# Optimization experiments

Hardware: AMD Instinct MI355X
Metric: run time of the kernel (lower is better)

The kernel has to match this reference:

```python
import jax, jax.numpy as jnp
import numpy as np

HEADS = 8
DIM_HEAD = 64
KERNEL = 33


def setup_inputs() -> dict:
    key = jax.random.key(0)
    k1, k2, k3 = jax.random.split(key, 3)
    b, n, dim = 8, 1315, 512
    x = jax.random.normal(k1, (b, n, dim), dtype=jnp.float32)
    w_qkv = jax.random.normal(k2, (dim, 3 * HEADS * DIM_HEAD), dtype=jnp.float32) * 0.02
    w_res = jax.random.normal(k3, (HEADS, 1, KERNEL, 1), dtype=jnp.float32) * 0.02
    return {"x": x, "w_qkv": w_qkv, "w_res": w_res,
            "target_num": 265, "neighbor_num": 25, "global_num": 1}


def reference(x, w_qkv, w_res, target_num, neighbor_num, global_num):
    b, n, _ = x.shape
    h, d = HEADS, DIM_HEAD
    scale = d ** -0.5
    num_image = target_num + neighbor_num + global_num

    qkv = x @ w_qkv                                   # [b, n, 3*h*d]
    q, k, v = jnp.split(qkv, 3, axis=-1)
    to_bhnd = lambda t: t.reshape(b, n, h, d).transpose(0, 2, 1, 3)
    q, k, v = map(to_bhnd, (q, k, v))                 # [b, h, n, d]
    q = q * scale

    q_img, k_img = q[:, :, :num_image], k[:, :, :num_image]
    q_gene, k_gene = q[:, :, num_image:], k[:, :, num_image:]

    cross_attn_image = jnp.einsum('bhid,bhjd->bhij', q_img, k_gene)   # [b,h,ni,ng]
    attn_gene = jnp.einsum('bhid,bhjd->bhij', q_gene, k_gene)          # [b,h,ng,ng]
    cross_attn_gene = jnp.einsum('bhid,bhjd->bhij', q_gene, k_img)     # [b,h,ng,ni]
    attn_image = jnp.einsum('bhid,bhjd->bhij', q_img, k_img)           # [b,h,ni,ni]

    # 'full' mode: softmax cross_attn_image first, then concatenated softmaxes
    cross_attn_image = jax.nn.softmax(cross_attn_image, axis=-1)
    attn_image_pathways = jax.nn.softmax(
        jnp.concatenate((cross_attn_image, attn_image), axis=-1), axis=-1)  # [b,h,ni,n]
    attn_gene_histology = jax.nn.softmax(
        jnp.concatenate((attn_gene, cross_attn_gene), axis=-1), axis=-1)    # [b,h,ng,n]

    out_pathways = attn_gene_histology @ v            # [b, h, ng, d]
    out_histology = attn_image_pathways @ v           # [b, h, ni, d]
    out = jnp.concatenate((out_pathways, out_histology), axis=2)  # [b, h, n, d]

    # depthwise residual conv over (n, d) with kernel (33, 1)
    pad = KERNEL // 2
    res = jax.lax.conv_general_dilated(
        v, w_res, window_strides=(1, 1), padding=((pad, pad), (0, 0)),
        dimension_numbers=('NCHW', 'OIHW', 'NCHW'), feature_group_count=h)
    out = out + res

    return out.transpose(0, 2, 1, 3).reshape(b, n, h * d)
```

## Files before the change

kernel.cpp:

```cpp
#include <hip/hip_runtime.h>

#define BATCH 8
#define NTOK 1315
#define DIM 512
#define HEADS 8
#define DH 64
#define NIMG 291
#define NGENE 1024
#define NQKV 1536
#define QSCALE 0.125f
#define KERN 33
#define NT 21
#define KROWS 1344
#define VROW 1392
#define VPAD 16
#define PLD 72

typedef float4 f4;
typedef __attribute__((ext_vector_type(8)))  short  short8;
typedef __attribute__((ext_vector_type(16))) float  fv16;
#define MFMA __builtin_amdgcn_mfma_f32_32x32x16_bf16

__device__ __forceinline__ ushort f2bf(float f) {
    union { float f; uint u; } v; v.f = f;
    uint u = v.u;
    uint r = u + 0x7FFFu + ((u >> 16) & 1u);
    return (ushort)(r >> 16);
}
__device__ __forceinline__ uint pack2(float a, float b) {
    return (uint)f2bf(a) | ((uint)f2bf(b) << 16);
}

__global__ __launch_bounds__(256) void prep(
    const float* __restrict__ w,
    ushort* __restrict__ kbb, ushort* __restrict__ vtb, ushort* __restrict__ wtb)
{
    const int step = gridDim.x * 256;
    const int tid0 = blockIdx.x * 256 + threadIdx.x;

    const int ktail = 64 * (KROWS - NTOK) * DH;
    for (int i = tid0; i < ktail; i += step) {
        int bh = i / ((KROWS - NTOK) * DH);
        int r  = i % ((KROWS - NTOK) * DH);
        kbb[(size_t)bh * KROWS * DH + (size_t)(NTOK + r / DH) * DH + (r % DH)] = 0;
    }
    const int vpadw = VPAD + (VROW - VPAD - NTOK);
    const int vtot = 64 * DH * vpadw;
    for (int i = tid0; i < vtot; i += step) {
        int row = i / vpadw, c = i % vpadw;
        int col = (c < VPAD) ? c : (VPAD + NTOK + (c - VPAD));
        vtb[(size_t)row * VROW + col] = 0;
    }
    const int wtot = NQKV * DIM;
    for (int i = tid0; i < wtot; i += step) {
        int k = i / NQKV, n = i - k * NQKV;
        wtb[(size_t)n * DIM + k] = f2bf(w[(size_t)k * NQKV + n]);
    }
}

__global__ __launch_bounds__(256) void qkv_gemm(
    const float* __restrict__ x, const ushort* __restrict__ wtb,
    ushort* __restrict__ qbb, ushort* __restrict__ kbb, ushort* __restrict__ vtb)
{
    __shared__ short As[128 * 64];
    __shared__ short Bsh[128 * 64];

    const int tid = threadIdx.x;
    const int lane = tid & 63;
    const int wv = tid >> 6;
    const int half = lane >> 5;
    const int ql = lane & 31;
    const int wy = wv >> 1, wx = wv & 1;
    const int b  = blockIdx.x / 11;
    const int m0 = (blockIdx.x % 11) * 128;
    const int n0 = blockIdx.y * 128;

    fv16 acc[2][2];
#pragma unroll
    for (int i = 0; i < 2; ++i)
#pragma unroll
        for (int j = 0; j < 2; ++j)
#pragma unroll
            for (int r = 0; r < 16; ++r) acc[i][j][r] = 0.f;

    for (int k0 = 0; k0 < DIM; k0 += 64) {
        __syncthreads();
#pragma unroll
        for (int u = 0; u < 4; ++u) {
            int i = u * 256 + tid, row = i >> 3, c = i & 7;
            int gm = m0 + row;
            f4 a0 = make_float4(0.f, 0.f, 0.f, 0.f), a1 = a0;
            if (gm < NTOK) {
                const float* xp = x + ((size_t)b * NTOK + gm) * DIM + k0 + c * 8;
                a0 = *(const f4*)xp;
                a1 = *(const f4*)(xp + 4);
            }
            uint4 p;
            p.x = pack2(a0.x, a0.y); p.y = pack2(a0.z, a0.w);
            p.z = pack2(a1.x, a1.y); p.w = pack2(a1.z, a1.w);
            *(uint4*)&As[row * 64 + 8 * (c ^ (row & 7))] = p;
        }
#pragma unroll
        for (int u = 0; u < 4; ++u) {
            int i = u * 256 + tid, row = i >> 3, c = i & 7;
            uint4 g = *(const uint4*)(wtb + (size_t)(n0 + row) * DIM + k0 + c * 8);
            *(uint4*)&Bsh[row * 64 + 8 * (c ^ (row & 7))] = g;
        }
        __syncthreads();
#pragma unroll
        for (int ki = 0; ki < 4; ++ki) {
            const int swz = ((ql & 7) << 3);
            const int off = (half * 8 + 16 * ki) ^ swz;
            short8 af0 = *(const short8*)&As[(wy * 64 + ql) * 64 + off];
            short8 af1 = *(const short8*)&As[(wy * 64 + 32 + ql) * 64 + off];
            short8 bf0 = *(const short8*)&Bsh[(wx * 64 + ql) * 64 + off];
            short8 bf1 = *(const short8*)&Bsh[(wx * 64 + 32 + ql) * 64 + off];
            acc[0][0] = MFMA(af0, bf0, acc[0][0], 0, 0, 0);
            acc[0][1] = MFMA(af0, bf1, acc[0][1], 0, 0, 0);
            acc[1][0] = MFMA(af1, bf0, acc[1][0], 0, 0, 0);
            acc[1][1] = MFMA(af1, bf1, acc[1][1], 0, 0, 0);
        }
    }

#pragma unroll
    for (int ri = 0; ri < 2; ++ri)
#pragma unroll
    for (int cj = 0; cj < 2; ++cj) {
        const int n = n0 + wx * 64 + cj * 32 + ql;
        const int which = n >> 9;
        const int hh = (n >> 6) & 7;
        const int dh = n & 63;
        const int bh = b * HEADS + hh;
        const int mb = m0 + wy * 64 + ri * 32 + 4 * half;
        if (which == 0) {
#pragma unroll
            for (int r = 0; r < 16; ++r) {
                int m = mb + (r & 3) + 8 * (r >> 2);
                if (m < NTOK)
                    qbb[((size_t)bh * NTOK + m) * DH + dh] = f2bf(acc[ri][cj][r] * QSCALE);
            }
        } else if (which == 1) {
#pragma unroll
            for (int r = 0; r < 16; ++r) {
                int m = mb + (r & 3) + 8 * (r >> 2);
                if (m < NTOK) {
                    int row = (m < NIMG) ? (m + NGENE) : (m - NIMG);
                    kbb[((size_t)bh * KROWS + row) * DH + dh] = f2bf(acc[ri][cj][r]);
                }
            }
        } else {
#pragma unroll
            for (int r = 0; r < 16; ++r) {
                int m = mb + (r & 3) + 8 * (r >> 2);
                if (m < NTOK)
                    vtb[((size_t)(bh * DH) + dh) * VROW + VPAD + m] = f2bf(acc[ri][cj][r]);
            }
        }
    }
}

__global__ __launch_bounds__(256) void attn_fused(
    const ushort* __restrict__ qbb, const ushort* __restrict__ kbb,
    const ushort* __restrict__ vtb, const float* __restrict__ wres,
    float* __restrict__ out)
{
    __shared__ short Kl[64 * 64];
    __shared__ short Pl[4][32 * PLD];

    const int tid = threadIdx.x;
    const int lane = tid & 63;
    const int wv = tid >> 6;
    const int half = lane >> 5;
    const int ql = lane & 31;
    const int bh = blockIdx.x, b = bh >> 3, h = bh & 7;
    const int cy = blockIdx.y;
    const bool isGene = cy < 8;
    const int orow0 = (isGene ? cy * 128 : NGENE + (cy - 8) * 128) + wv * 32;
    const int orow_q = orow0 + ql;
    int qtok = isGene ? (NIMG + orow_q) : (orow_q - NGENE);
    if (!isGene && qtok >= NIMG) qtok = 0;

    short8 qf[4];
    {
        const ushort* qrow = qbb + ((size_t)bh * NTOK + qtok) * DH;
#pragma unroll
        for (int ki = 0; ki < 4; ++ki)
            qf[ki] = *(const short8*)(qrow + half * 8 + 16 * ki);
    }
    short8 tf[4];
    {
        const float* wr = wres + h * KERN;
#pragma unroll
        for (int ki = 0; ki < 4; ++ki) {
            short8 v;
#pragma unroll
            for (int e = 0; e < 8; ++e) {
                int k = half * 8 + e + 16 * ki;
                int t = k - ql;
                float wl = (t >= 0 && t <= 32) ? wr[t] : 0.f;
                v[e] = (short)f2bf(wl);
            }
            tf[ki] = v;
        }
    }

    const size_t kbase = (size_t)bh * KROWS * DH;

#define STAGE(tile) {                                                          \
        int i0 = tid,       j0 = i0 >> 3, c0 = i0 & 7;                         \
        int i1 = 256 + tid, j1 = i1 >> 3, c1 = i1 & 7;                         \
        uint4 g0 = *(const uint4*)(kbb + kbase + (size_t)((tile)*64 + j0) * DH + c0 * 8); \
        uint4 g1 = *(const uint4*)(kbb + kbase + (size_t)((tile)*64 + j1) * DH + c1 * 8); \
        *(uint4*)&Kl[j0 * 64 + 8 * (c0 ^ (j0 & 7))] = g0;                      \
        *(uint4*)&Kl[j1 * 64 + 8 * (c1 ^ (j1 & 7))] = g1;                      \
    }
#define QKT(s0v, s1v) {                                                        \
        _Pragma("unroll")                                                      \
        for (int r = 0; r < 16; ++r) { s0v[r] = 0.f; s1v[r] = 0.f; }           \
        _Pragma("unroll")                                                      \
        for (int ki = 0; ki < 4; ++ki) {                                       \
            int off = (half * 8 + 16 * ki) ^ ((ql & 7) << 3);                  \
            short8 a0 = *(const short8*)&Kl[ql * 64 + off];                    \
            short8 a1 = *(const short8*)&Kl[(32 + ql) * 64 + off];             \
            s0v = MFMA(a0, qf[ki], s0v, 0, 0, 0);                              \
            s1v = MFMA(a1, qf[ki], s1v, 0, 0, 0);                              \
        }                                                                      \
    }
#define MASK_LAST(s1v) {                                                       \
        _Pragma("unroll")                                                      \
        for (int r = 0; r < 16; ++r) {                                         \
            int off = (r & 3) + 8 * (r >> 2) + 4 * half;                       \
            if (off >= 3) s1v[r] = -1e30f;          \
        }                                                                      \
    }
#define TILEMAX(s0v, s1v, tm) {                                                \
        float ta = -1e30f, tb = -1e30f;                                        \
        _Pragma("unroll")                                                      \
        for (int r = 0; r < 16; r += 2) {                                      \
            ta = fmaxf(ta, fmaxf(s0v[r], s0v[r + 1]));                         \
            tb = fmaxf(tb, fmaxf(s1v[r], s1v[r + 1]));                         \
        }                                                                      \
        tm = fmaxf(ta, tb);                                                    \
        tm = fmaxf(tm, __shfl_xor(tm, 32, 64));                                \
    }
#define PV(p0, p1, t064, O0, O1) {                                             \
        _Pragma("unroll")                                                      \
        for (int i = 0; i < 4; ++i) {                                          \
            uint2 w0; w0.x = pack2(p0[4*i], p0[4*i+1]); w0.y = pack2(p0[4*i+2], p0[4*i+3]); \
            *(uint2*)&Pl[wv][ql * PLD + 8 * i + 4 * half] = w0;                \
            uint2 w1; w1.x = pack2(p1[4*i], p1[4*i+1]); w1.y = pack2(p1[4*i+2], p1[4*i+3]); \
            *(uint2*)&Pl[wv][ql * PLD + 32 + 8 * i + 4 * half] = w1;           \
        }                                                                      \
        const ushort* vr0 = vtb + ((size_t)(bh * DH) + ql) * VROW + VPAD + (t064); \
        const ushort* vr1 = vr0 + (size_t)32 * VROW;                           \
        _Pragma("unroll")                                                      \
        for (int ki = 0; ki < 4; ++ki) {                                       \
            short8 pa = *(const short8*)&Pl[wv][ql * PLD + half * 8 + 16 * ki]; \
            short8 v0 = *(const short8*)(vr0 + half * 8 + 16 * ki);            \
            short8 v1 = *(const short8*)(vr1 + half * 8 + 16 * ki);            \
            O0 = MFMA(pa, v0, O0, 0, 0, 0);                                    \
            O1 = MFMA(pa, v1, O1, 0, 0, 0);                                    \
        }                                                                      \
    }
#define SCALE_O(val, O0, O1) {                                                 \
        _Pragma("unroll")                                                      \
        for (int r = 0; r < 16; ++r) {                                         \
            int qm = (r & 3) + 8 * (r >> 2) + 4 * half;                        \
            float c = __shfl(val, qm, 64);                                     \
            O0[r] *= c; O1[r] *= c;                                            \
        }                                                                      \
    }

    fv16 O0, O1;
#pragma unroll
    for (int r = 0; r < 16; ++r) { O0[r] = 0.f; O1[r] = 0.f; }

    if (isGene) {
        float m = -1e30f, ss = 0.f;
        for (int t = 0; t < NT; ++t) {
            __syncthreads();
            STAGE(t);
            __syncthreads();
            fv16 s0v, s1v;
            QKT(s0v, s1v);
            if (t == NT - 1) MASK_LAST(s1v);
            float tm; TILEMAX(s0v, s1v, tm);
            if (__any(tm > m)) {
                float mn = fmaxf(m, tm);
                float corr = __expf(m - mn);
                ss *= corr;
                SCALE_O(corr, O0, O1);
                m = mn;
            }
#pragma unroll
            for (int r = 0; r < 16; ++r) {
                s0v[r] = __expf(s0v[r] - m); ss += s0v[r];
                s1v[r] = __expf(s1v[r] - m); ss += s1v[r];
            }
            PV(s0v, s1v, t * 64, O0, O1);
        }
        float sf = ss + __shfl_xor(ss, 32, 64);
        float inv = 1.0f / sf;
        SCALE_O(inv, O0, O1);
    } else {
        float m1 = -1e30f, s1s = 0.f, m2 = -1e30f;
        for (int t = 0; t < NT; ++t) {
            __syncthreads();
            STAGE(t);
            __syncthreads();
            fv16 s0v, s1v;
            QKT(s0v, s1v);
            if (t == NT - 1) MASK_LAST(s1v);
            float tm; TILEMAX(s0v, s1v, tm);
            if (t < 16) {
                if (__any(tm > m1)) {
                    float mn = fmaxf(m1, tm);
                    s1s *= __expf(m1 - mn);
                    m1 = mn;
                }
#pragma unroll
                for (int r = 0; r < 16; ++r)
                    s1s += __expf(s0v[r] - m1) + __expf(s1v[r] - m1);
            } else {
                m2 = fmaxf(m2, tm);
            }
        }
        s1s += __shfl_xor(s1s, 32, 64);
        float invs1 = 1.0f / s1s;
        float M = fmaxf(invs1, m2);
        float Z = 0.f;
        for (int t = 0; t < NT; ++t) {
            __syncthreads();
            STAGE(t);
            __syncthreads();
            fv16 s0v, s1v;
            QKT(s0v, s1v);
            if (t == NT - 1) MASK_LAST(s1v);
            if (t < 16) {
#pragma unroll
                for (int r = 0; r < 16; ++r) {
                    s0v[r] = __expf(__expf(s0v[r] - m1) * invs1 - M); Z += s0v[r];
                    s1v[r] = __expf(__expf(s1v[r] - m1) * invs1 - M); Z += s1v[r];
                }
            } else {
#pragma unroll
                for (int r = 0; r < 16; ++r) {
                    s0v[r] = __expf(s0v[r] - M); Z += s0v[r];
                    s1v[r] = __expf(s1v[r] - M); Z += s1v[r];
                }
            }
            PV(s0v, s1v, t * 64, O0, O1);
        }
        float Zf = Z + __shfl_xor(Z, 32, 64);
        float inv = 1.0f / Zf;
        SCALE_O(inv, O0, O1);
    }

    if (isGene || orow0 < NTOK) {
        {
            const ushort* cr0 = vtb + ((size_t)(bh * DH) + ql) * VROW + orow0;
            const ushort* cr1 = cr0 + (size_t)32 * VROW;
#pragma unroll
            for (int ki = 0; ki < 4; ++ki) {
                short8 v0 = *(const short8*)(cr0 + half * 8 + 16 * ki);
                short8 v1 = *(const short8*)(cr1 + half * 8 + 16 * ki);
                O0 = MFMA(tf[ki], v0, O0, 0, 0, 0);
                O1 = MFMA(tf[ki], v1, O1, 0, 0, 0);
            }
        }
#pragma unroll
        for (int r = 0; r < 16; ++r) {
            int qm = (r & 3) + 8 * (r >> 2) + 4 * half;
            int orow = orow0 + qm;
            if (isGene || orow < NTOK) {
                float* op = out + ((size_t)b * NTOK + orow) * DIM + h * DH + ql;
                op[0]  = O0[r];
                op[32] = O1[r];
            }
        }
    }
#undef STAGE
#undef QKT
#undef MASK_LAST
#undef TILEMAX
#undef PV
#undef SCALE_O
}

extern "C" void kernel_launch(void* const* d_in, const int* in_sizes, int n_in,
                              void* d_out, int out_size, void* d_ws, size_t ws_size,
                              hipStream_t stream)
{
    const float* x     = (const float*)d_in[0];
    const float* w_qkv = (const float*)d_in[1];
    const float* w_res = (const float*)d_in[2];
    float* out = (float*)d_out;

    const size_t qElems = (size_t)BATCH * HEADS * NTOK * DH;
    const size_t kElems = (size_t)BATCH * HEADS * KROWS * DH;
    const size_t vElems = (size_t)BATCH * HEADS * DH * VROW;
    ushort* qbb = (ushort*)d_ws;
    ushort* kbb = qbb + qElems;
    ushort* vtb = kbb + kElems;
    ushort* wtb = vtb + vElems;

    prep<<<dim3(256), 256, 0, stream>>>(w_qkv, kbb, vtb, wtb);
    qkv_gemm<<<dim3(BATCH * 11, NQKV / 128), 256, 0, stream>>>(x, wtb, qbb, kbb, vtb);
    attn_fused<<<dim3(BATCH * HEADS, 11), 256, 0, stream>>>(qbb, kbb, vtb, w_res, out);
}
```

Before: 262.8 us.

## Prefetch K tiles, use exp2 softmax, tiled weight/V transposes, hw bf16 pack

```diff
diff --git a/kernel.cpp b/kernel.cpp
--- a/kernel.cpp
+++ b/kernel.cpp
@@ -8,13 +8,14 @@
 #define NIMG 291
 #define NGENE 1024
 #define NQKV 1536
-#define QSCALE 0.125f
 #define KERN 33
 #define NT 21
 #define KROWS 1344
 #define VROW 1392
 #define VPAD 16
 #define PLD 72
+#define LAM 1.4426950408889634f
+#define QL2 (0.125f * LAM)
 
 typedef float4 f4;
 typedef __attribute__((ext_vector_type(8)))  short  short8;
@@ -27,40 +28,69 @@
     uint r = u + 0x7FFFu + ((u >> 16) & 1u);
     return (ushort)(r >> 16);
 }
-__device__ __forceinline__ uint pack2(float a, float b) {
-    return (uint)f2bf(a) | ((uint)f2bf(b) << 16);
-}
-
-__global__ __launch_bounds__(256) void prep(
-    const float* __restrict__ w,
-    ushort* __restrict__ kbb, ushort* __restrict__ vtb, ushort* __restrict__ wtb)
+__device__ __forceinline__ uint cvtpk(float lo, float hi) {
+    uint r;
+    asm("v_cvt_pk_bf16_f32 %0, %1, %2" : "=v"(r) : "v"(lo), "v"(hi));
+    return r;
+}
+__device__ __forceinline__ float ex2(float x) {
+    float r;
+    asm("v_exp_f32 %0, %1" : "=v"(r) : "v"(x));
+    return r;
+}
+
+__global__ __launch_bounds__(256) void prep_zero(
+    ushort* __restrict__ kbb, ushort* __restrict__ vtb)
 {
     const int step = gridDim.x * 256;
     const int tid0 = blockIdx.x * 256 + threadIdx.x;
-
     const int ktail = 64 * (KROWS - NTOK) * DH;
     for (int i = tid0; i < ktail; i += step) {
         int bh = i / ((KROWS - NTOK) * DH);
         int r  = i % ((KROWS - NTOK) * DH);
         kbb[(size_t)bh * KROWS * DH + (size_t)(NTOK + r / DH) * DH + (r % DH)] = 0;
     }
-    const int vpadw = VPAD + (VROW - VPAD - NTOK);
+    const int rz = VROW - (VPAD + 1344);
+    const int vpadw = VPAD + rz;
     const int vtot = 64 * DH * vpadw;
     for (int i = tid0; i < vtot; i += step) {
         int row = i / vpadw, c = i % vpadw;
-        int col = (c < VPAD) ? c : (VPAD + NTOK + (c - VPAD));
+        int col = (c < VPAD) ? c : (VPAD + 1344 + (c - VPAD));
         vtb[(size_t)row * VROW + col] = 0;
     }
-    const int wtot = NQKV * DIM;
-    for (int i = tid0; i < wtot; i += step) {
-        int k = i / NQKV, n = i - k * NQKV;
-        wtb[(size_t)n * DIM + k] = f2bf(w[(size_t)k * NQKV + n]);
+}
+
+__global__ __launch_bounds__(256) void wtrans(
+    const float* __restrict__ w, ushort* __restrict__ wtb)
+{
+    __shared__ short T[64][72];
+    const int n0 = blockIdx.x * 64;
+    const int k0 = blockIdx.y * 64;
+    const int tid = threadIdx.x;
+    {
+        int kr = tid >> 2, c0 = (tid & 3) * 16;
+        const float* src = w + (size_t)(k0 + kr) * NQKV + n0 + c0;
+#pragma unroll
+        for (int j = 0; j < 16; j += 4) {
+            f4 v = *(const f4*)(src + j);
+            T[c0 + j + 0][kr] = (short)f2bf(v.x);
+            T[c0 + j + 1][kr] = (short)f2bf(v.y);
+            T[c0 + j + 2][kr] = (short)f2bf(v.z);
+            T[c0 + j + 3][kr] = (short)f2bf(v.w);
+        }
+    }
+    __syncthreads();
+    {
+        int nr = tid >> 2, c0 = (tid & 3) * 16;
+        ushort* dst = wtb + (size_t)(n0 + nr) * DIM + k0 + c0;
+        *(short8*)dst       = *(const short8*)&T[nr][c0];
+        *(short8*)(dst + 8) = *(const short8*)&T[nr][c0 + 8];
     }
 }
 
 __global__ __launch_bounds__(256) void qkv_gemm(
     const float* __restrict__ x, const ushort* __restrict__ wtb,
-    ushort* __restrict__ qbb, ushort* __restrict__ kbb, ushort* __restrict__ vtb)
+    ushort* __restrict__ qbb, ushort* __restrict__ kbb, ushort* __restrict__ vnb)
 {
     __shared__ short As[128 * 64];
     __shared__ short Bsh[128 * 64];
@@ -96,8 +126,8 @@
                 a1 = *(const f4*)(xp + 4);
             }
             uint4 p;
-            p.x = pack2(a0.x, a0.y); p.y = pack2(a0.z, a0.w);
-            p.z = pack2(a1.x, a1.y); p.w = pack2(a1.z, a1.w);
+            p.x = cvtpk(a0.x, a0.y); p.y = cvtpk(a0.z, a0.w);
+            p.z = cvtpk(a1.x, a1.y); p.w = cvtpk(a1.z, a1.w);
             *(uint4*)&As[row * 64 + 8 * (c ^ (row & 7))] = p;
         }
 #pragma unroll
@@ -109,8 +139,7 @@
         __syncthreads();
 #pragma unroll
         for (int ki = 0; ki < 4; ++ki) {
-            const int swz = ((ql & 7) << 3);
-            const int off = (half * 8 + 16 * ki) ^ swz;
+            const int off = (half * 8 + 16 * ki) ^ ((ql & 7) << 3);
             short8 af0 = *(const short8*)&As[(wy * 64 + ql) * 64 + off];
             short8 af1 = *(const short8*)&As[(wy * 64 + 32 + ql) * 64 + off];
             short8 bf0 = *(const short8*)&Bsh[(wx * 64 + ql) * 64 + off];
@@ -137,7 +166,7 @@
             for (int r = 0; r < 16; ++r) {
                 int m = mb + (r & 3) + 8 * (r >> 2);
                 if (m < NTOK)
-                    qbb[((size_t)bh * NTOK + m) * DH + dh] = f2bf(acc[ri][cj][r] * QSCALE);
+                    qbb[((size_t)bh * NTOK + m) * DH + dh] = f2bf(acc[ri][cj][r] * QL2);
             }
         } else if (which == 1) {
 #pragma unroll
@@ -153,9 +182,39 @@
             for (int r = 0; r < 16; ++r) {
                 int m = mb + (r & 3) + 8 * (r >> 2);
                 if (m < NTOK)
-                    vtb[((size_t)(bh * DH) + dh) * VROW + VPAD + m] = f2bf(acc[ri][cj][r]);
-            }
-        }
+                    vnb[((size_t)bh * NTOK + m) * DH + dh] = f2bf(acc[ri][cj][r]);
+            }
+        }
+    }
+}
+
+__global__ __launch_bounds__(256) void vtrans(
+    const ushort* __restrict__ vnb, ushort* __restrict__ vtb)
+{
+    __shared__ short T[64][72];
+    const int bh = blockIdx.x;
+    const int t0 = blockIdx.y * 64;
+    const int tid = threadIdx.x;
+    {
+        int tr = tid >> 2, d0 = (tid & 3) * 16;
+        int tok = t0 + tr;
+        short8 a, c;
+#pragma unroll
+        for (int e = 0; e < 8; ++e) { a[e] = 0; c[e] = 0; }
+        if (tok < NTOK) {
+            const ushort* src = vnb + ((size_t)bh * NTOK + tok) * DH + d0;
+            a = *(const short8*)src;
+            c = *(const short8*)(src + 8);
+        }
+#pragma unroll
+        for (int e = 0; e < 8; ++e) { T[d0 + e][tr] = a[e]; T[d0 + 8 + e][tr] = c[e]; }
+    }
+    __syncthreads();
+    {
+        int dr = tid >> 2, c0 = (tid & 3) * 16;
+        ushort* dst = vtb + ((size_t)(bh * DH) + dr) * VROW + VPAD + t0 + c0;
+        *(short8*)dst       = *(const short8*)&T[dr][c0];
+        *(short8*)(dst + 8) = *(const short8*)&T[dr][c0 + 8];
     }
 }
 
@@ -174,8 +233,8 @@
     const int ql = lane & 31;
     const int bh = blockIdx.x, b = bh >> 3, h = bh & 7;
     const int cy = blockIdx.y;
-    const bool isGene = cy < 8;
-    const int orow0 = (isGene ? cy * 128 : NGENE + (cy - 8) * 128) + wv * 32;
+    const bool isGene = cy >= 3;
+    const int orow0 = (isGene ? (cy - 3) * 128 : NGENE + cy * 128) + wv * 32;
     const int orow_q = orow0 + ql;
     int qtok = isGene ? (NIMG + orow_q) : (orow_q - NGENE);
     if (!isGene && qtok >= NIMG) qtok = 0;
@@ -205,14 +264,19 @@
     }
 
     const size_t kbase = (size_t)bh * KROWS * DH;
-
-#define STAGE(tile) {                                                          \
+    uint4 sg0, sg1;
+
+#define STAGE_LOAD(tile) {                                                     \
         int i0 = tid,       j0 = i0 >> 3, c0 = i0 & 7;                         \
         int i1 = 256 + tid, j1 = i1 >> 3, c1 = i1 & 7;                         \
-        uint4 g0 = *(const uint4*)(kbb + kbase + (size_t)((tile)*64 + j0) * DH + c0 * 8); \
-        uint4 g1 = *(const uint4*)(kbb + kbase + (size_t)((tile)*64 + j1) * DH + c1 * 8); \
-        *(uint4*)&Kl[j0 * 64 + 8 * (c0 ^ (j0 & 7))] = g0;                      \
-        *(uint4*)&Kl[j1 * 64 + 8 * (c1 ^ (j1 & 7))] = g1;                      \
+        sg0 = *(const uint4*)(kbb + kbase + (size_t)((tile)*64 + j0) * DH + c0 * 8); \
+        sg1 = *(const uint4*)(kbb + kbase + (size_t)((tile)*64 + j1) * DH + c1 * 8); \
+    }
+#define STAGE_WRITE() {                                                        \
+        int i0 = tid,       j0 = i0 >> 3, c0 = i0 & 7;                         \
+        int i1 = 256 + tid, j1 = i1 >> 3, c1 = i1 & 7;                         \
+        *(uint4*)&Kl[j0 * 64 + 8 * (c0 ^ (j0 & 7))] = sg0;                     \
+        *(uint4*)&Kl[j1 * 64 + 8 * (c1 ^ (j1 & 7))] = sg1;                     \
     }
 #define QKT(s0v, s1v) {                                                        \
         _Pragma("unroll")                                                      \
@@ -246,9 +310,9 @@
 #define PV(p0, p1, t064, O0, O1) {                                             \
         _Pragma("unroll")                                                      \
         for (int i = 0; i < 4; ++i) {                                          \
-            uint2 w0; w0.x = pack2(p0[4*i], p0[4*i+1]); w0.y = pack2(p0[4*i+2], p0[4*i+3]); \
+            uint2 w0; w0.x = cvtpk(p0[4*i], p0[4*i+1]); w0.y = cvtpk(p0[4*i+2], p0[4*i+3]); \
             *(uint2*)&Pl[wv][ql * PLD + 8 * i + 4 * half] = w0;                \
-            uint2 w1; w1.x = pack2(p1[4*i], p1[4*i+1]); w1.y = pack2(p1[4*i+2], p1[4*i+3]); \
+            uint2 w1; w1.x = cvtpk(p1[4*i], p1[4*i+1]); w1.y = cvtpk(p1[4*i+2], p1[4*i+3]); \
             *(uint2*)&Pl[wv][ql * PLD + 32 + 8 * i + 4 * half] = w1;           \
         }                                                                      \
         const ushort* vr0 = vtb + ((size_t)(bh * DH) + ql) * VROW + VPAD + (t064); \
@@ -277,79 +341,90 @@
 
     if (isGene) {
         float m = -1e30f, ss = 0.f;
+        STAGE_LOAD(0); STAGE_WRITE(); __syncthreads();
         for (int t = 0; t < NT; ++t) {
-            __syncthreads();
-            STAGE(t);
-            __syncthreads();
+            const bool more = (t + 1 < NT);
+            if (more) STAGE_LOAD(t + 1);
             fv16 s0v, s1v;
             QKT(s0v, s1v);
+            __syncthreads();
+            if (more) STAGE_WRITE();
             if (t == NT - 1) MASK_LAST(s1v);
             float tm; TILEMAX(s0v, s1v, tm);
             if (__any(tm > m)) {
                 float mn = fmaxf(m, tm);
-                float corr = __expf(m - mn);
+                float corr = ex2(m - mn);
                 ss *= corr;
                 SCALE_O(corr, O0, O1);
                 m = mn;
             }
 #pragma unroll
             for (int r = 0; r < 16; ++r) {
-                s0v[r] = __expf(s0v[r] - m); ss += s0v[r];
-                s1v[r] = __expf(s1v[r] - m); ss += s1v[r];
+                s0v[r] = ex2(s0v[r] - m); ss += s0v[r];
+                s1v[r] = ex2(s1v[r] - m); ss += s1v[r];
             }
             PV(s0v, s1v, t * 64, O0, O1);
+            __syncthreads();
         }
         float sf = ss + __shfl_xor(ss, 32, 64);
         float inv = 1.0f / sf;
         SCALE_O(inv, O0, O1);
     } else {
-        float m1 = -1e30f, s1s = 0.f, m2 = -1e30f;
+        float m1 = -1e30f, s1s = 0.f, m2p = -1e30f;
+        STAGE_LOAD(0); STAGE_WRITE(); __syncthreads();
         for (int t = 0; t < NT; ++t) {
-            __syncthreads();
-            STAGE(t);
-            __syncthreads();
+            const bool more = (t + 1 < NT);
+            if (more) STAGE_LOAD(t + 1);
             fv16 s0v, s1v;
             QKT(s0v, s1v);
+            __syncthreads();
+            if (more) STAGE_WRITE();
             if (t == NT - 1) MASK_LAST(s1v);
             float tm; TILEMAX(s0v, s1v, tm);
             if (t < 16) {
                 if (__any(tm > m1)) {
                     float mn = fmaxf(m1, tm);
-                    s1s *= __expf(m1 - mn);
+                    s1s *= ex2(m1 - mn);
                     m1 = mn;
                 }
 #pragma unroll
                 for (int r = 0; r < 16; ++r)
-                    s1s += __expf(s0v[r] - m1) + __expf(s1v[r] - m1);
+                    s1s += ex2(s0v[r] - m1) + ex2(s1v[r] - m1);
             } else {
-                m2 = fmaxf(m2, tm);
-            }
+                m2p = fmaxf(m2p, tm);
+            }
+            __syncthreads();
         }
         s1s += __shfl_xor(s1s, 32, 64);
         float invs1 = 1.0f / s1s;
-        float M = fmaxf(invs1, m2);
+        float c1 = __log2f(LAM * invs1);
+        float m1c = m1 - c1;
+        float M2 = fmaxf(LAM * invs1, m2p);
         float Z = 0.f;
+        STAGE_LOAD(0); STAGE_WRITE(); __syncthreads();
         for (int t = 0; t < NT; ++t) {
-            __syncthreads();
-            STAGE(t);
-            __syncthreads();
+            const bool more = (t + 1 < NT);
+            if (more) STAGE_LOAD(t + 1);
             fv16 s0v, s1v;
             QKT(s0v, s1v);
+            __syncthreads();
+            if (more) STAGE_WRITE();
             if (t == NT - 1) MASK_LAST(s1v);
             if (t < 16) {
 #pragma unroll
                 for (int r = 0; r < 16; ++r) {
-                    s0v[r] = __expf(__expf(s0v[r] - m1) * invs1 - M); Z += s0v[r];
-                    s1v[r] = __expf(__expf(s1v[r] - m1) * invs1 - M); Z += s1v[r];
+                    s0v[r] = ex2(ex2(s0v[r] - m1c) - M2); Z += s0v[r];
+                    s1v[r] = ex2(ex2(s1v[r] - m1c) - M2); Z += s1v[r];
                 }
             } else {
 #pragma unroll
                 for (int r = 0; r < 16; ++r) {
-                    s0v[r] = __expf(s0v[r] - M); Z += s0v[r];
-                    s1v[r] = __expf(s1v[r] - M); Z += s1v[r];
+                    s0v[r] = ex2(s0v[r] - M2); Z += s0v[r];
+                    s1v[r] = ex2(s1v[r] - M2); Z += s1v[r];
                 }
             }
             PV(s0v, s1v, t * 64, O0, O1);
+            __syncthreads();
         }
         float Zf = Z + __shfl_xor(Z, 32, 64);
         float inv = 1.0f / Zf;
@@ -379,7 +454,8 @@
             }
         }
     }
-#undef STAGE
+#undef STAGE_LOAD
+#undef STAGE_WRITE
 #undef QKT
 #undef MASK_LAST
 #undef TILEMAX
@@ -401,10 +477,13 @@
     const size_t vElems = (size_t)BATCH * HEADS * DH * VROW;
     ushort* qbb = (ushort*)d_ws;
     ushort* kbb = qbb + qElems;
-    ushort* vtb = kbb + kElems;
+    ushort* vnb = kbb + kElems;
+    ushort* vtb = vnb + qElems;
     ushort* wtb = vtb + vElems;
 
-    prep<<<dim3(256), 256, 0, stream>>>(w_qkv, kbb, vtb, wtb);
-    qkv_gemm<<<dim3(BATCH * 11, NQKV / 128), 256, 0, stream>>>(x, wtb, qbb, kbb, vtb);
+    prep_zero<<<dim3(64), 256, 0, stream>>>(kbb, vtb);
+    wtrans<<<dim3(NQKV / 64, DIM / 64), 256, 0, stream>>>(w_qkv, wtb);
+    qkv_gemm<<<dim3(BATCH * 11, NQKV / 128), 256, 0, stream>>>(x, wtb, qbb, kbb, vnb);
+    vtrans<<<dim3(BATCH * HEADS, NT), 256, 0, stream>>>(vnb, vtb);
     attn_fused<<<dim3(BATCH * HEADS, 11), 256, 0, stream>>>(qbb, kbb, vtb, w_res, out);
 }
```

After: 234.7 us. -10.7%, faster.
